# Optimization experiments

Hardware: AMD Instinct MI355X
Metric: run time of the kernel (lower is better)

Reference implementation:

```python
import jax, jax.numpy as jnp
import numpy as np

NS, NV = 48, 10                    # scalar / vector multiplicities (cfg.ns, cfg.nv)
WN = NS * NS + NS * NV             # per-edge TP weight numel: paths 0e*0e->0e and 0e*1o->1o
OUT = NS + 3 * NV                  # out irreps 48x0e + 10x1o -> 78 dims
INV = float(1.0 / np.sqrt(NS))     # e3nn-style path normalization (fan_in = mul_in)
N_LIG, N_REC, N_ATOM = 2000, 2000, 15000
E_LL, E_RR, E_AA = 15000, 10000, 15000
E_LR, E_LA, E_AR = 5000, 8000, 8000


def setup_inputs() -> dict:
    key = jax.random.key(0)
    ks = jax.random.split(key, 40)
    f = lambda i, shape, s=1.0: jax.random.normal(ks[i], shape, dtype=jnp.float32) * s
    ii = lambda i, n, e: jax.random.randint(ks[i], (e,), 0, n, dtype=jnp.int32)
    w_s = (1.0 / (3 * NS)) ** 0.5
    return {
        'lig_x': f(0, (N_LIG, NS)), 'rec_x': f(1, (N_REC, NS)), 'atom_x': f(2, (N_ATOM, NS)),
        'll_attr': f(3, (E_LL, NS)), 'rr_attr': f(4, (E_RR, NS)), 'aa_attr': f(5, (E_AA, NS)),
        'lr_attr': f(6, (E_LR, NS)), 'la_attr': f(7, (E_LA, NS)), 'ar_attr': f(8, (E_AR, NS)),
        'll_sh': f(9, (E_LL, 9)), 'rr_sh': f(10, (E_RR, 9)), 'aa_sh': f(11, (E_AA, 9)),
        'lr_sh': f(12, (E_LR, 9)), 'la_sh': f(13, (E_LA, 9)), 'ar_sh': f(14, (E_AR, 9)),
        'mlp_w1': f(15, (9, 3 * NS, 3 * NS), w_s), 'mlp_b1': jnp.zeros((9, 3 * NS), jnp.float32),
        'mlp_w2': f(16, (9, 3 * NS, 3 * NS), w_s), 'mlp_b2': jnp.zeros((9, 3 * NS), jnp.float32),
        'mlp_w3': f(17, (9, 3 * NS, WN), w_s), 'mlp_b3': jnp.zeros((9, WN), jnp.float32),
        'll_src': ii(18, N_LIG, E_LL), 'll_dst': ii(19, N_LIG, E_LL),
        'rr_src': ii(20, N_REC, E_RR), 'rr_dst': ii(21, N_REC, E_RR),
        'aa_src': ii(22, N_ATOM, E_AA), 'aa_dst': ii(23, N_ATOM, E_AA),
        'lr_lig': ii(24, N_LIG, E_LR), 'lr_rec': ii(25, N_REC, E_LR),
        'la_lig': ii(26, N_LIG, E_LA), 'la_atom': ii(27, N_ATOM, E_LA),
        'ar_atom': ii(28, N_ATOM, E_AR), 'ar_rec': ii(29, N_REC, E_AR),
    }


def _tp_conv(src_x, dst_x, e_attr, e_sh, src_idx, dst_idx, n_dst, w1, b1, w2, b2, w3, b3):
    """FullyConnectedTensorProductConv: per-edge MLP -> TP weights, CG tensor
    product of gathered source features with edge SH, mean scatter to dst."""
    fs = src_x[src_idx]                                          # (E, ns) gather
    z = jnp.concatenate([e_attr, fs, dst_x[dst_idx]], axis=-1)
    h = jax.nn.relu(z @ w1 + b1)
    h = jax.nn.relu(h @ w2 + b2)
    w = h @ w3 + b3                                              # (E, WN) edge-conditioned TP weights
    w0 = w[:, : NS * NS].reshape(-1, NS, NS)                     # 0e x 0e -> 0e path
    wv = w[:, NS * NS :].reshape(-1, NS, NV)                     # 0e x 1o -> 1o path
    out0 = jnp.einsum('ei,eio->eo', fs, w0) * e_sh[:, :1] * INV  # (E, ns)
    outv = jnp.einsum('ei,eiv,em->evm', fs, wv, e_sh[:, 1:4]) * INV  # (E, nv, 3)
    msg = jnp.concatenate([out0, outv.reshape(-1, NV * 3)], axis=-1)
    agg = jax.ops.segment_sum(msg, dst_idx, num_segments=n_dst)
    deg = jax.ops.segment_sum(jnp.ones((msg.shape[0], 1), msg.dtype), dst_idx, num_segments=n_dst)
    return agg / jnp.maximum(deg, 1.0)                           # mean reduction


def reference(lig_x, rec_x, atom_x, ll_attr, rr_attr, aa_attr, lr_attr, la_attr, ar_attr,
              ll_sh, rr_sh, aa_sh, lr_sh, la_sh, ar_sh,
              mlp_w1, mlp_b1, mlp_w2, mlp_b2, mlp_w3, mlp_b3,
              ll_src, ll_dst, rr_src, rr_dst, aa_src, aa_dst,
              lr_lig, lr_rec, la_lig, la_atom, ar_atom, ar_rec):
    P = lambda c: (mlp_w1[c], mlp_b1[c], mlp_w2[c], mlp_b2[c], mlp_w3[c], mlp_b3[c])
    # one interaction layer = 9 structurally distinct convs (lig/rec/atom intra + 6 cross dirs)
    lig_u = (_tp_conv(lig_x, lig_x, ll_attr, ll_sh, ll_src, ll_dst, N_LIG, *P(0))
           + _tp_conv(rec_x, lig_x, lr_attr, lr_sh, lr_rec, lr_lig, N_LIG, *P(1))
           + _tp_conv(atom_x, lig_x, la_attr, la_sh, la_atom, la_lig, N_LIG, *P(2)))
    rec_u = (_tp_conv(lig_x, rec_x, lr_attr, lr_sh, lr_lig, lr_rec, N_REC, *P(3))
           + _tp_conv(rec_x, rec_x, rr_attr, rr_sh, rr_src, rr_dst, N_REC, *P(4))
           + _tp_conv(atom_x, rec_x, ar_attr, ar_sh, ar_atom, ar_rec, N_REC, *P(5)))
    atom_u = (_tp_conv(lig_x, atom_x, la_attr, la_sh, la_lig, la_atom, N_ATOM, *P(6))
            + _tp_conv(rec_x, atom_x, ar_attr, ar_sh, ar_rec, ar_atom, N_ATOM, *P(7))
            + _tp_conv(atom_x, atom_x, aa_attr, aa_sh, aa_src, aa_dst, N_ATOM, *P(8)))
    pad = lambda x: jnp.pad(x, ((0, 0), (0, OUT - NS)))          # residual: pad scalars to out irreps
    return jnp.concatenate([pad(lig_x) + lig_u, pad(rec_x) + rec_u, pad(atom_x) + atom_u], axis=0)
```

## Files before the change

### kernel.cpp

```cpp
#include <hip/hip_runtime.h>


namespace {

constexpr int NCONV = 9;
constexpr int ETOT  = 82000;
constexpr float INV = 0.14433756729740643f;

constexpr int EC[NCONV]     = {15000,5000,8000,5000,10000,8000,8000,8000,15000};
constexpr int NBLKC[NCONV]  = {118,40,63,40,79,63,63,63,118};
constexpr int EOFF[NCONV]   = {0,15000,20000,28000,33000,43000,51000,59000,67000};
constexpr int DEGOFF[NCONV] = {0,2000,4000,6000,8000,10000,12000,27000,42000};
constexpr int NODEC[NCONV]  = {2000,2000,2000,2000,2000,2000,15000,15000,15000};
constexpr int NBLK_TOT = 647;

typedef _Float16 f16;
typedef __attribute__((ext_vector_type(8))) _Float16 f16x8;
typedef __attribute__((ext_vector_type(4))) _Float16 f16x4;
typedef __attribute__((ext_vector_type(4))) float f32x4;

#define MFMA(a, b, c) __builtin_amdgcn_mfma_f32_16x16x32_f16((a), (b), (c), 0, 0, 0)

struct ConvPtrs {
  const float* src_x[NCONV];
  const float* dst_x[NCONV];
  const float* attr[NCONV];
  const float* sh[NCONV];
  const int*   sidx[NCONV];
  const int*   didx[NCONV];
};

}

__device__ __forceinline__ int SW(int idx) { return idx ^ ((idx >> 3) & 3); }

__device__ __forceinline__ int xcd_remap(int bid) {
  const int xcd = bid & 7, slot = bid >> 3;
  return (xcd <= 6) ? (xcd * 81 + slot) : (567 + slot);
}

__device__ __forceinline__ int conv_decode(int bid, int& rem) {
  int c = 0; rem = bid;
  while (c < NCONV - 1 && rem >= NBLKC[c]) { rem -= NBLKC[c]; ++c; }
  return c;
}

__device__ __forceinline__ void gld_lds16(const void* g, void* l) {
  __builtin_amdgcn_global_load_lds(
      (const __attribute__((address_space(1))) void*)g,
      (__attribute__((address_space(3))) void*)l, 16, 0, 0);
}

__global__ __launch_bounds__(256) void prep_all(
    ConvPtrs P,
    const float* __restrict__ w1, const float* __restrict__ b1,
    const float* __restrict__ w2, const float* __restrict__ b2,
    const float* __restrict__ w3, const float* __restrict__ b3,
    f16* __restrict__ w1f, f16* __restrict__ w2f, f16* __restrict__ w3f,
    float* __restrict__ deg) {
  __shared__ float W[145][60];
  const int blk = blockIdx.x;
  if (blk < 203) {
    const int unit = blk * 4 + (threadIdx.x >> 6);
    if (unit >= 810) return;
    const int l = threadIdx.x & 63;
    const int sel = unit >= 405, bb = sel ? unit - 405 : unit;
    const int c = bb / 45, r2 = bb % 45, cb = r2 / 5, s = r2 % 5;
    const float* w  = sel ? w2 : w1;
    const float* bi = sel ? b2 : b1;
    f16* dst = (sel ? w2f : w1f) + ((size_t)(c * 9 + cb) * 5 + s) * 512;
    const int n = cb * 16 + (l & 15);
    f16x8 pack;
#pragma unroll
    for (int j = 0; j < 8; ++j) {
      const int k = s * 32 + ((l >> 4) << 3) + j;
      float v = 0.f;
      if (k < 144)       v = w[((size_t)c * 144 + k) * 144 + n];
      else if (k == 144) v = bi[c * 144 + n];
      pack[j] = (f16)v;
    }
    ((f16x8*)dst)[l] = pack;
  } else if (blk < 635) {
    const int b = blk - 203;
    const int c = b / 48, i = b % 48;
    const float* wc = w3 + (size_t)c * 144 * 2784;
    const float* bc = b3 + (size_t)c * 2784;
    for (int u = threadIdx.x; u < 145 * 58; u += 256) {
      const int row = u / 58, t = u - row * 58;
      const int col = (t < 48) ? (i * 48 + t) : (2304 + i * 10 + (t - 48));
      const float* src = (row == 144) ? bc : (wc + (size_t)row * 2784);
      W[row][t] = src[col];
    }
    __syncthreads();
    f16* dst = w3f + (size_t)(c * 48 + i) * 20 * 512;
#pragma unroll
    for (int it = 0; it < 5; ++it) {
      const int f8 = it * 256 + threadIdx.x;
      const int s = f8 >> 8, g2 = f8 & 255, cb = g2 >> 6, l = g2 & 63;
      const int k0 = s * 32 + ((l >> 4) << 3);
      const int col = cb * 16 + (l & 15);
      f16x8 pack;
#pragma unroll
      for (int j = 0; j < 8; ++j) {
        const int k = k0 + j;
        pack[j] = (f16)((k <= 144 && col < 58) ? W[k][col] : 0.f);
      }
      ((f16x8*)dst)[f8] = pack;
    }
  } else {
    const int gid = (blk - 635) * 256 + threadIdx.x;
    if (gid >= ETOT) return;
    int c = 0;
    while (c < NCONV - 1 && gid >= EOFF[c + 1]) ++c;
    const int e = gid - EOFF[c];
    atomicAdd(&deg[DEGOFF[c] + P.didx[c][e]], 1.0f);
  }
}

__global__ __launch_bounds__(256) void scan_kernel(
    const float* __restrict__ deg, int* __restrict__ offs, int* __restrict__ cursor) {
  __shared__ int part[256];
  const int c = blockIdx.x, N = NODEC[c], base = DEGOFF[c];
  const int tid = threadIdx.x;
  const int chunk = (N + 255) / 256;
  const int start = tid * chunk;
  const int end = (start + chunk < N) ? (start + chunk) : N;
  int s = 0;
  for (int i = start; i < end; ++i) s += (int)deg[base + i];
  part[tid] = s;
  __syncthreads();
  if (tid == 0) {
    int acc = 0;
    for (int k = 0; k < 256; ++k) { int t = part[k]; part[k] = acc; acc += t; }
  }
  __syncthreads();
  int acc = part[tid];
  for (int i = start; i < end; ++i) {
    offs[base + i] = acc; cursor[base + i] = acc;
    acc += (int)deg[base + i];
  }
}

__global__ __launch_bounds__(256) void slot_kernel(
    ConvPtrs P, int* __restrict__ cursor, int* __restrict__ inv_slot) {
  const int gid = blockIdx.x * 256 + threadIdx.x;
  if (gid >= ETOT) return;
  int c = 0;
  while (c < NCONV - 1 && gid >= EOFF[c + 1]) ++c;
  const int e = gid - EOFF[c];
  const int d = P.didx[c][e];
  inv_slot[gid] = atomicAdd(&cursor[DEGOFF[c] + d], 1);
}

template<int NCB, int CB0>
__device__ __forceinline__ void layer_mm(
    const f16x8* __restrict__ Av, const f16x8* __restrict__ wv,
    int c, int lane, int lane_sw, int wr, f32x4 acc[4][5]) {
#pragma unroll
  for (int rb = 0; rb < 4; ++rb)
#pragma unroll
    for (int cb = 0; cb < NCB; ++cb) acc[rb][cb] = (f32x4)0.0f;
#pragma unroll
  for (int s = 0; s < 5; ++s) {
    f16x8 B[NCB];
#pragma unroll
    for (int cb = 0; cb < NCB; ++cb)
      B[cb] = wv[((size_t)(c * 9 + CB0 + cb) * 5 + s) * 64 + lane];
    f16x8 A[4];
#pragma unroll
    for (int rb = 0; rb < 4; ++rb) A[rb] = Av[((wr * 4 + rb) * 5 + s) * 64 + lane_sw];
#pragma unroll
    for (int rb = 0; rb < 4; ++rb)
#pragma unroll
      for (int cb = 0; cb < NCB; ++cb)
        acc[rb][cb] = MFMA(A[rb], B[cb], acc[rb][cb]);
  }
}

template<int NCB, int CB0>
__device__ __forceinline__ void layer_wb(const f32x4 acc[4][5], f16* __restrict__ At,
                                         int lane, int wr) {
#pragma unroll
  for (int cb = 0; cb < NCB; ++cb) {
    const int k = (CB0 + cb) * 16 + (lane & 15);
    const int s = k >> 5, g = (k >> 3) & 3, j = k & 7;
#pragma unroll
    for (int rb = 0; rb < 4; ++rb)
#pragma unroll
      for (int r = 0; r < 4; ++r) {
        const int row = ((lane >> 4) << 2) + r;
        const int sf = (wr * 4 + rb) * 5 + s;
        At[(sf * 64 + SW(g * 16 + row)) * 8 + j] =
            (f16)fmaxf(acc[rb][cb][r], 0.f);
      }
  }
}

__global__ __launch_bounds__(256)
__attribute__((amdgpu_waves_per_eu(3, 3)))
void mlp_kernel(
    ConvPtrs P, const f16* __restrict__ w1f, const f16* __restrict__ w2f,
    f16* __restrict__ h2g, f16* __restrict__ fstg) {
  __shared__ __align__(16) char smem[54272];
  f16* Atile = (f16*)smem;
  f16 (*fst)[48] = (f16 (*)[48])(smem + 40960);
  int* sidb = (int*)(smem + 53248);
  int* dstb = (int*)(smem + 53760);

  const int f = xcd_remap(blockIdx.x);
  int rem; const int c = conv_decode(f, rem);
  const int E = EC[c], e0 = rem * 128;
  const int tid = threadIdx.x, lane = tid & 63, w = tid >> 6;
  const int wr = w >> 1, wc = w & 1;
  const int lane_sw = SW(lane);

  if (tid < 128) {
    int ec = e0 + tid; if (ec >= E) ec = E - 1;
    sidb[tid] = P.sidx[c][ec];
    dstb[tid] = P.didx[c][ec];
  }
  __syncthreads();

  {
    const float* attr = P.attr[c];
    const float* sx = P.src_x[c];
    const float* dx = P.dst_x[c];
#pragma unroll
    for (int it = 0; it < 10; ++it) {
      const int u = it * 256 + tid, j8 = u >> 7, e = u & 127;
      int ec = e0 + e; if (ec >= E) ec = E - 1;
      const float* p;
      if (j8 < 6)       p = attr + (size_t)ec * 48 + j8 * 8;
      else if (j8 < 12) p = sx + (size_t)sidb[e] * 48 + (j8 - 6) * 8;
      else if (j8 < 18) p = dx + (size_t)dstb[e] * 48 + (j8 - 12) * 8;
      else              p = attr;
      const f32x4 va = *(const f32x4*)p;
      const f32x4 vb = *(const f32x4*)(p + 4);
      float v[8];
#pragma unroll
      for (int t = 0; t < 4; ++t) { v[t] = va[t]; v[4 + t] = vb[t]; }
      if (j8 == 18) {
        v[0] = 1.f;
#pragma unroll
        for (int t = 1; t < 8; ++t) v[t] = 0.f;
      } else if (j8 == 19) {
#pragma unroll
        for (int t = 0; t < 8; ++t) v[t] = 0.f;
      }
      f16x8 h;
#pragma unroll
      for (int t = 0; t < 8; ++t) h[t] = (f16)v[t];
      if (j8 >= 6 && j8 < 12) {
        *(f16x8*)&fst[e][(j8 - 6) * 8] = h;
      }
      const int s = j8 >> 2, g = j8 & 3, rbg = e >> 4, row = e & 15;
      ((f16x8*)Atile)[(rbg * 5 + s) * 64 + SW(g * 16 + row)] = h;
    }
  }
  __syncthreads();

  const f16x8* Av = (const f16x8*)Atile;
  f32x4 acc[4][5];
  if (wc == 0) layer_mm<5, 0>(Av, (const f16x8*)w1f, c, lane, lane_sw, wr, acc);
  else         layer_mm<4, 5>(Av, (const f16x8*)w1f, c, lane, lane_sw, wr, acc);
  __syncthreads();
  if (wc == 0) layer_wb<5, 0>(acc, Atile, lane, wr);
  else         layer_wb<4, 5>(acc, Atile, lane, wr);
  __syncthreads();
  if (wc == 0) layer_mm<5, 0>(Av, (const f16x8*)w2f, c, lane, lane_sw, wr, acc);
  else         layer_mm<4, 5>(Av, (const f16x8*)w2f, c, lane, lane_sw, wr, acc);
  __syncthreads();
  if (wc == 0) layer_wb<5, 0>(acc, Atile, lane, wr);
  else         layer_wb<4, 5>(acc, Atile, lane, wr);
  __syncthreads();

  const f16x8* As = (const f16x8*)Atile;
  f16x8* hd = (f16x8*)(h2g + (size_t)f * 20480);
#pragma unroll
  for (int t = 0; t < 10; ++t) hd[t * 256 + tid] = As[t * 256 + tid];
  const f16x8* fs8 = (const f16x8*)fst;
  f16x8* fd = (f16x8*)(fstg + (size_t)f * 6144);
#pragma unroll
  for (int t = 0; t < 3; ++t) fd[t * 256 + tid] = fs8[t * 256 + tid];
}

__device__ __forceinline__ void bilin_step2(
    const f16* __restrict__ slot, const f16 (*fstl)[48], int i,
    const f16x8 Af[4][5], f32x4 msg[4][2], int lane, int wr, int wc) {
  f16x8 fsv[4];
#pragma unroll
  for (int rb = 0; rb < 4; ++rb) {
    const f16 fs = fstl[(wr * 4 + rb) * 16 + (lane & 15)][i];
#pragma unroll
    for (int t = 0; t < 8; ++t) fsv[rb][t] = fs;
  }
  const f16x8* bv = (const f16x8*)slot;
  __builtin_amdgcn_s_setprio(1);
#pragma unroll
  for (int s = 0; s < 5; ++s) {
    const f16x8 Bf0 = bv[(s * 4 + wc * 2 + 0) * 64 + lane];
    const f16x8 Bf1 = bv[(s * 4 + wc * 2 + 1) * 64 + lane];
#pragma unroll
    for (int rb = 0; rb < 4; ++rb) {
      const f16x8 a = Af[rb][s] * fsv[rb];
      msg[rb][0] = MFMA(a, Bf0, msg[rb][0]);
      msg[rb][1] = MFMA(a, Bf1, msg[rb][1]);
    }
  }
  __builtin_amdgcn_s_setprio(0);
}

__global__ __launch_bounds__(256)
__attribute__((amdgpu_waves_per_eu(3, 3)))
void bilin_kernel(
    ConvPtrs P, const f16* __restrict__ w3f, const f16* __restrict__ h2g,
    const f16* __restrict__ fstg, const float* __restrict__ deg,
    const int* __restrict__ inv_slot, f16* __restrict__ medge) {
  __shared__ __align__(16) char smem[53248];
  f16* ring = (f16*)smem;
  f16 (*fstl)[48] = (f16 (*)[48])(smem + 40960);

  const int f = xcd_remap(blockIdx.x);
  int rem; const int c = conv_decode(f, rem);
  const int E = EC[c], e0 = rem * 128;
  const int tid = threadIdx.x, lane = tid & 63, w = tid >> 6;
  const int wr = w >> 1, wc = w & 1;
  const int lane_sw = SW(lane);

  const f16x8* hv = (const f16x8*)(h2g + (size_t)f * 20480);
  f16x8 Af[4][5];
#pragma unroll
  for (int rb = 0; rb < 4; ++rb)
#pragma unroll
    for (int s = 0; s < 5; ++s)
      Af[rb][s] = hv[((wr * 4 + rb) * 5 + s) * 64 + lane_sw];

  const f16* fsrc = fstg + (size_t)f * 6144;
#pragma unroll
  for (int t = 0; t < 3; ++t) {
    const int chunk = w * 3 + t;
    gld_lds16(fsrc + chunk * 512 + lane * 8, ((f16*)fstl) + chunk * 512);
  }
  const f16* __restrict__ w3c = w3f + (size_t)(c * 48) * 10240;
#pragma unroll
  for (int q = 0; q < 5; ++q) {
    const int chunk = q * 4 + w;
    gld_lds16(w3c + chunk * 512 + lane * 8, ring + chunk * 512);
  }

  f32x4 msg[4][2];
#pragma unroll
  for (int rb = 0; rb < 4; ++rb)
#pragma unroll
    for (int cb = 0; cb < 2; ++cb) msg[rb][cb] = (f32x4)0.0f;

#pragma unroll 1
  for (int i = 0; i < 47; ++i) {
    __builtin_amdgcn_s_barrier();
    const f16* gsrc = w3c + (size_t)(i + 1) * 10240;
    f16* bdst = ring + ((i + 1) & 1) * 10240;
#pragma unroll
    for (int q = 0; q < 5; ++q) {
      const int chunk = q * 4 + w;
      gld_lds16(gsrc + chunk * 512 + lane * 8, bdst + chunk * 512);
    }
    asm volatile("s_waitcnt vmcnt(5)" ::: "memory");
    __builtin_amdgcn_s_barrier();
    __builtin_amdgcn_sched_barrier(0);
    bilin_step2(ring + (i & 1) * 10240, fstl, i, Af, msg, lane, wr, wc);
  }
  __builtin_amdgcn_s_barrier();
  asm volatile("s_waitcnt vmcnt(0)" ::: "memory");
  __builtin_amdgcn_s_barrier();
  bilin_step2(ring + (47 & 1) * 10240, fstl, 47, Af, msg, lane, wr, wc);

  const float* __restrict__ shp = P.sh[c];
  const float* __restrict__ degc = deg + DEGOFF[c];
  const int* __restrict__ didx = P.didx[c];
#pragma unroll
  for (int rb = 0; rb < 4; ++rb)
#pragma unroll
    for (int r = 0; r < 4; ++r) {
      const int el = wr * 64 + rb * 16 + ((lane >> 4) << 2) + r;
      const int ec = e0 + el;
      if (ec >= E) continue;
      const float sc = INV / fmaxf(degc[didx[ec]], 1.f);
      const float* shq = shp + (size_t)ec * 9;
      const float s0 = shq[0], s1 = shq[1], s2 = shq[2], s3 = shq[3];
      const int pos = inv_slot[EOFF[c] + ec];
      f16* mp = medge + (size_t)(EOFF[c] + pos) * 80;
#pragma unroll
      for (int cb = 0; cb < 2; ++cb) {
        const int col = (wc * 2 + cb) * 16 + (lane & 15);
        const float v = msg[rb][cb][r] * sc;
        if (col < 48) {
          mp[col] = (f16)(v * s0);
        } else if (col < 58) {
          const int vv = col - 48;
          mp[48 + vv * 3 + 0] = (f16)(v * s1);
          mp[48 + vv * 3 + 1] = (f16)(v * s2);
          mp[48 + vv * 3 + 2] = (f16)(v * s3);
        }
      }
    }
}

__global__ __launch_bounds__(256) void finalize_kernel(
    const float* __restrict__ lig, const float* __restrict__ rec,
    const float* __restrict__ atom, const int* __restrict__ offs,
    const int* __restrict__ cursor, const f16* __restrict__ medge,
    float* __restrict__ out) {
  const int tid = threadIdx.x;
  if (tid >= 240) return;
  const int r3 = tid / 80, j = tid - r3 * 80;
  const int row = blockIdx.x * 3 + r3;
  if (row >= 19000 || j >= 78) return;
  int node, cb; const float* x;
  if (row < 2000)      { node = row;        cb = 0; x = lig; }
  else if (row < 4000) { node = row - 2000; cb = 3; x = rec; }
  else                 { node = row - 4000; cb = 6; x = atom; }
  float r = (j < 48) ? x[(size_t)node * 48 + j] : 0.f;
#pragma unroll
  for (int t = 0; t < 3; ++t) {
    const int c = cb + t;
    const int base = DEGOFF[c] + node;
    const int o = offs[base], e = cursor[base];
    for (int k = o; k < e; ++k)
      r += (float)medge[(size_t)(EOFF[c] + k) * 80 + j];
  }
  out[(size_t)row * 78 + j] = r;
}

extern "C" void kernel_launch(void* const* d_in, const int* in_sizes, int n_in,
                              void* d_out, int out_size, void* d_ws, size_t ws_size,
                              hipStream_t stream) {
  (void)in_sizes; (void)n_in; (void)out_size; (void)ws_size;
  const float* lig_x  = (const float*)d_in[0];
  const float* rec_x  = (const float*)d_in[1];
  const float* atom_x = (const float*)d_in[2];
  const float* attr_ll = (const float*)d_in[3];
  const float* attr_rr = (const float*)d_in[4];
  const float* attr_aa = (const float*)d_in[5];
  const float* attr_lr = (const float*)d_in[6];
  const float* attr_la = (const float*)d_in[7];
  const float* attr_ar = (const float*)d_in[8];
  const float* sh_ll = (const float*)d_in[9];
  const float* sh_rr = (const float*)d_in[10];
  const float* sh_aa = (const float*)d_in[11];
  const float* sh_lr = (const float*)d_in[12];
  const float* sh_la = (const float*)d_in[13];
  const float* sh_ar = (const float*)d_in[14];
  const float* w1 = (const float*)d_in[15];
  const float* b1 = (const float*)d_in[16];
  const float* w2 = (const float*)d_in[17];
  const float* b2 = (const float*)d_in[18];
  const float* w3 = (const float*)d_in[19];
  const float* b3 = (const float*)d_in[20];
  const int* ll_src = (const int*)d_in[21];
  const int* ll_dst = (const int*)d_in[22];
  const int* rr_src = (const int*)d_in[23];
  const int* rr_dst = (const int*)d_in[24];
  const int* aa_src = (const int*)d_in[25];
  const int* aa_dst = (const int*)d_in[26];
  const int* lr_lig = (const int*)d_in[27];
  const int* lr_rec = (const int*)d_in[28];
  const int* la_lig = (const int*)d_in[29];
  const int* la_atom = (const int*)d_in[30];
  const int* ar_atom = (const int*)d_in[31];
  const int* ar_rec  = (const int*)d_in[32];

  f16* w1f = (f16*)d_ws;
  f16* w2f = w1f + 207360;
  f16* w3f = w2f + 207360;
  float* deg     = (float*)(w3f + 4423680);
  int*   offs    = (int*)(deg + 57000);
  int*   cursor  = offs + 57000;
  int*   inv_slot= cursor + 57000;
  f16*   medge   = (f16*)(inv_slot + 82000);
  f16*   h2g     = medge + 6560000;
  f16*   fstg    = h2g + 13250560;

  ConvPtrs P;
  const float* SX[NCONV] = {lig_x, rec_x, atom_x, lig_x, rec_x, atom_x, lig_x, rec_x, atom_x};
  const float* DX[NCONV] = {lig_x, lig_x, lig_x, rec_x, rec_x, rec_x, atom_x, atom_x, atom_x};
  const float* AT[NCONV] = {attr_ll, attr_lr, attr_la, attr_lr, attr_rr, attr_ar, attr_la, attr_ar, attr_aa};
  const float* SH[NCONV] = {sh_ll, sh_lr, sh_la, sh_lr, sh_rr, sh_ar, sh_la, sh_ar, sh_aa};
  const int*   SI[NCONV] = {ll_src, lr_rec, la_atom, lr_lig, rr_src, ar_atom, la_lig, ar_rec, aa_src};
  const int*   DI[NCONV] = {ll_dst, lr_lig, la_lig, lr_rec, rr_dst, ar_rec, la_atom, ar_atom, aa_dst};
  for (int cc = 0; cc < NCONV; ++cc) {
    P.src_x[cc] = SX[cc]; P.dst_x[cc] = DX[cc]; P.attr[cc] = AT[cc];
    P.sh[cc] = SH[cc]; P.sidx[cc] = SI[cc]; P.didx[cc] = DI[cc];
  }

  hipMemsetAsync(deg, 0, 57000 * sizeof(float), stream);
  prep_all<<<956, 256, 0, stream>>>(P, w1, b1, w2, b2, w3, b3, w1f, w2f, w3f, deg);
  scan_kernel<<<NCONV, 256, 0, stream>>>(deg, offs, cursor);
  slot_kernel<<<(ETOT + 255) / 256, 256, 0, stream>>>(P, cursor, inv_slot);
  mlp_kernel<<<NBLK_TOT, 256, 0, stream>>>(P, w1f, w2f, h2g, fstg);
  bilin_kernel<<<NBLK_TOT, 256, 0, stream>>>(P, w3f, h2g, fstg, deg, inv_slot, medge);
  finalize_kernel<<<(19000 + 2) / 3, 256, 0, stream>>>(lig_x, rec_x, atom_x, offs,
                                                       cursor, medge, (float*)d_out);
}
```

Before: 193.0 us.

## Merge pairs of bilinear tiles into 512-thread blocks sharing the W3 ring

The bilinear kernel now processes two 128-edge tiles per 512-thread block, so each streamed 48-slice W3 weight ring in LDS serves 256 edges instead of 128. This halves the number of blocks and the global/L2 traffic for W3 loads. Only five waves issue the async loads, and the rest wait on vmcnt(0). LDS per block rises to 64 KB and waves_per_eu changes to 4, which alters occupancy. The odd-count tail reuses a duplicated tile index, and the hidden epilogue must handle it correctly.

```diff
diff --git a/kernel.cpp b/kernel.cpp
--- a/kernel.cpp
+++ b/kernel.cpp
@@ -9,14 +9,16 @@
 
 constexpr int EC[NCONV]     = {15000,5000,8000,5000,10000,8000,8000,8000,15000};
 constexpr int NBLKC[NCONV]  = {118,40,63,40,79,63,63,63,118};
+constexpr int TOFF[NCONV]   = {0,118,158,221,261,340,403,466,529};
+constexpr int NBLKC2[NCONV] = {59,20,32,20,40,32,32,32,59};
 constexpr int EOFF[NCONV]   = {0,15000,20000,28000,33000,43000,51000,59000,67000};
 constexpr int DEGOFF[NCONV] = {0,2000,4000,6000,8000,10000,12000,27000,42000};
 constexpr int NODEC[NCONV]  = {2000,2000,2000,2000,2000,2000,15000,15000,15000};
 constexpr int NBLK_TOT = 647;
+constexpr int NBLK2_TOT = 326;
 
 typedef _Float16 f16;
 typedef __attribute__((ext_vector_type(8))) _Float16 f16x8;
-typedef __attribute__((ext_vector_type(4))) _Float16 f16x4;
 typedef __attribute__((ext_vector_type(4))) float f32x4;
 
 #define MFMA(a, b, c) __builtin_amdgcn_mfma_f32_16x16x32_f16((a), (b), (c), 0, 0, 0)
@@ -38,10 +40,19 @@
   const int xcd = bid & 7, slot = bid >> 3;
   return (xcd <= 6) ? (xcd * 81 + slot) : (567 + slot);
 }
+__device__ __forceinline__ int xcd_remap326(int bid) {
+  const int xcd = bid & 7, slot = bid >> 3;
+  return (xcd < 6) ? (xcd * 41 + slot) : (246 + (xcd - 6) * 40 + slot);
+}
 
 __device__ __forceinline__ int conv_decode(int bid, int& rem) {
   int c = 0; rem = bid;
   while (c < NCONV - 1 && rem >= NBLKC[c]) { rem -= NBLKC[c]; ++c; }
+  return c;
+}
+__device__ __forceinline__ int conv_decode2(int bid, int& rem) {
+  int c = 0; rem = bid;
+  while (c < NCONV - 1 && rem >= NBLKC2[c]) { rem -= NBLKC2[c]; ++c; }
   return c;
 }
 
@@ -290,7 +301,7 @@
   f16x8 fsv[4];
 #pragma unroll
   for (int rb = 0; rb < 4; ++rb) {
-    const f16 fs = fstl[(wr * 4 + rb) * 16 + (lane & 15)][i];
+    const f16 fs = fstl[wr * 64 + rb * 16 + (lane & 15)][i];
 #pragma unroll
     for (int t = 0; t < 8; ++t) fsv[rb][t] = fs;
   }
@@ -310,42 +321,51 @@
   __builtin_amdgcn_s_setprio(0);
 }
 
-__global__ __launch_bounds__(256)
-__attribute__((amdgpu_waves_per_eu(3, 3)))
+__global__ __launch_bounds__(512)
+__attribute__((amdgpu_waves_per_eu(4, 4)))
 void bilin_kernel(
     ConvPtrs P, const f16* __restrict__ w3f, const f16* __restrict__ h2g,
     const f16* __restrict__ fstg, const float* __restrict__ deg,
     const int* __restrict__ inv_slot, f16* __restrict__ medge) {
-  __shared__ __align__(16) char smem[53248];
+  __shared__ __align__(16) char smem[65536];
   f16* ring = (f16*)smem;
   f16 (*fstl)[48] = (f16 (*)[48])(smem + 40960);
 
-  const int f = xcd_remap(blockIdx.x);
-  int rem; const int c = conv_decode(f, rem);
-  const int E = EC[c], e0 = rem * 128;
+  const int fb = xcd_remap326(blockIdx.x);
+  int rem; const int c = conv_decode2(fb, rem);
+  const int E = EC[c], e0 = rem * 256;
   const int tid = threadIdx.x, lane = tid & 63, w = tid >> 6;
   const int wr = w >> 1, wc = w & 1;
   const int lane_sw = SW(lane);
 
-  const f16x8* hv = (const f16x8*)(h2g + (size_t)f * 20480);
+  const int tcnt = NBLKC[c];
+  const int tg0 = TOFF[c] + 2 * rem;
+  const int tg1 = TOFF[c] + ((2 * rem + 1 < tcnt) ? (2 * rem + 1) : (tcnt - 1));
+  const int tgw = (wr >> 1) ? tg1 : tg0;
+  const int hb  = wr & 1;
+
+  const f16x8* hv = (const f16x8*)(h2g + (size_t)tgw * 20480);
   f16x8 Af[4][5];
 #pragma unroll
   for (int rb = 0; rb < 4; ++rb)
 #pragma unroll
     for (int s = 0; s < 5; ++s)
-      Af[rb][s] = hv[((wr * 4 + rb) * 5 + s) * 64 + lane_sw];
-
-  const f16* fsrc = fstg + (size_t)f * 6144;
+      Af[rb][s] = hv[((hb * 4 + rb) * 5 + s) * 64 + lane_sw];
+
 #pragma unroll
   for (int t = 0; t < 3; ++t) {
     const int chunk = w * 3 + t;
-    gld_lds16(fsrc + chunk * 512 + lane * 8, ((f16*)fstl) + chunk * 512);
+    const int tg = (chunk >= 12) ? tg1 : tg0;
+    const f16* src = fstg + (size_t)tg * 6144 + (chunk % 12) * 512;
+    gld_lds16(src + lane * 8, ((f16*)fstl) + chunk * 512);
   }
   const f16* __restrict__ w3c = w3f + (size_t)(c * 48) * 10240;
-#pragma unroll
-  for (int q = 0; q < 5; ++q) {
-    const int chunk = q * 4 + w;
-    gld_lds16(w3c + chunk * 512 + lane * 8, ring + chunk * 512);
+  if (w < 5) {
+#pragma unroll
+    for (int q = 0; q < 4; ++q) {
+      const int chunk = w * 4 + q;
+      gld_lds16(w3c + chunk * 512 + lane * 8, ring + chunk * 512);
+    }
   }
 
   f32x4 msg[4][2];
@@ -357,14 +377,18 @@
 #pragma unroll 1
   for (int i = 0; i < 47; ++i) {
     __builtin_amdgcn_s_barrier();
-    const f16* gsrc = w3c + (size_t)(i + 1) * 10240;
-    f16* bdst = ring + ((i + 1) & 1) * 10240;
-#pragma unroll
-    for (int q = 0; q < 5; ++q) {
-      const int chunk = q * 4 + w;
-      gld_lds16(gsrc + chunk * 512 + lane * 8, bdst + chunk * 512);
-    }
-    asm volatile("s_waitcnt vmcnt(5)" ::: "memory");
+    if (w < 5) {
+      const f16* gsrc = w3c + (size_t)(i + 1) * 10240;
+      f16* bdst = ring + ((i + 1) & 1) * 10240;
+#pragma unroll
+      for (int q = 0; q < 4; ++q) {
+        const int chunk = w * 4 + q;
+        gld_lds16(gsrc + chunk * 512 + lane * 8, bdst + chunk * 512);
+      }
+      asm volatile("s_waitcnt vmcnt(4)" ::: "memory");
+    } else {
+      asm volatile("s_waitcnt vmcnt(0)" ::: "memory");
+    }
     __builtin_amdgcn_s_barrier();
     __builtin_amdgcn_sched_barrier(0);
     bilin_step2(ring + (i & 1) * 10240, fstl, i, Af, msg, lane, wr, wc);
@@ -497,7 +521,7 @@
   scan_kernel<<<NCONV, 256, 0, stream>>>(deg, offs, cursor);
   slot_kernel<<<(ETOT + 255) / 256, 256, 0, stream>>>(P, cursor, inv_slot);
   mlp_kernel<<<NBLK_TOT, 256, 0, stream>>>(P, w1f, w2f, h2g, fstg);
-  bilin_kernel<<<NBLK_TOT, 256, 0, stream>>>(P, w3f, h2g, fstg, deg, inv_slot, medge);
+  bilin_kernel<<<NBLK2_TOT, 512, 0, stream>>>(P, w3f, h2g, fstg, deg, inv_slot, medge);
   finalize_kernel<<<(19000 + 2) / 3, 256, 0, stream>>>(lig_x, rec_x, atom_x, offs,
                                                        cursor, medge, (float*)d_out);
 }
```

After: 219.9 us. 13.9% more time.

## Load bilinear weight fragments directly from global instead of LDS ring

Applied to the files above, without the earlier changes.

Replaces the double-buffered LDS ring, which staged per-step w3 weight slices with async global-to-LDS copies and barriers, with direct per-wave global loads of the B fragments into registers, unrolled by two. This drops the per-iteration block barriers and most LDS usage, which should raise achievable occupancy. The waves_per_eu pin is also removed. The trade is that latency hiding now relies on the compiler's unrolled loads and cache hits, and each wave now fetches its weight slice from global/L2 itself rather than through the shared LDS copy.

```diff
diff --git a/kernel.cpp b/kernel.cpp
--- a/kernel.cpp
+++ b/kernel.cpp
@@ -16,7 +16,6 @@
 
 typedef _Float16 f16;
 typedef __attribute__((ext_vector_type(8))) _Float16 f16x8;
-typedef __attribute__((ext_vector_type(4))) _Float16 f16x4;
 typedef __attribute__((ext_vector_type(4))) float f32x4;
 
 #define MFMA(a, b, c) __builtin_amdgcn_mfma_f32_16x16x32_f16((a), (b), (c), 0, 0, 0)
@@ -284,41 +283,12 @@
   for (int t = 0; t < 3; ++t) fd[t * 256 + tid] = fs8[t * 256 + tid];
 }
 
-__device__ __forceinline__ void bilin_step2(
-    const f16* __restrict__ slot, const f16 (*fstl)[48], int i,
-    const f16x8 Af[4][5], f32x4 msg[4][2], int lane, int wr, int wc) {
-  f16x8 fsv[4];
-#pragma unroll
-  for (int rb = 0; rb < 4; ++rb) {
-    const f16 fs = fstl[(wr * 4 + rb) * 16 + (lane & 15)][i];
-#pragma unroll
-    for (int t = 0; t < 8; ++t) fsv[rb][t] = fs;
-  }
-  const f16x8* bv = (const f16x8*)slot;
-  __builtin_amdgcn_s_setprio(1);
-#pragma unroll
-  for (int s = 0; s < 5; ++s) {
-    const f16x8 Bf0 = bv[(s * 4 + wc * 2 + 0) * 64 + lane];
-    const f16x8 Bf1 = bv[(s * 4 + wc * 2 + 1) * 64 + lane];
-#pragma unroll
-    for (int rb = 0; rb < 4; ++rb) {
-      const f16x8 a = Af[rb][s] * fsv[rb];
-      msg[rb][0] = MFMA(a, Bf0, msg[rb][0]);
-      msg[rb][1] = MFMA(a, Bf1, msg[rb][1]);
-    }
-  }
-  __builtin_amdgcn_s_setprio(0);
-}
-
 __global__ __launch_bounds__(256)
-__attribute__((amdgpu_waves_per_eu(3, 3)))
 void bilin_kernel(
     ConvPtrs P, const f16* __restrict__ w3f, const f16* __restrict__ h2g,
     const f16* __restrict__ fstg, const float* __restrict__ deg,
     const int* __restrict__ inv_slot, f16* __restrict__ medge) {
-  __shared__ __align__(16) char smem[53248];
-  f16* ring = (f16*)smem;
-  f16 (*fstl)[48] = (f16 (*)[48])(smem + 40960);
+  __shared__ __align__(16) f16 fstl[128][48];
 
   const int f = xcd_remap(blockIdx.x);
   int rem; const int c = conv_decode(f, rem);
@@ -341,12 +311,7 @@
     const int chunk = w * 3 + t;
     gld_lds16(fsrc + chunk * 512 + lane * 8, ((f16*)fstl) + chunk * 512);
   }
-  const f16* __restrict__ w3c = w3f + (size_t)(c * 48) * 10240;
-#pragma unroll
-  for (int q = 0; q < 5; ++q) {
-    const int chunk = q * 4 + w;
-    gld_lds16(w3c + chunk * 512 + lane * 8, ring + chunk * 512);
-  }
+  __syncthreads();
 
   f32x4 msg[4][2];
 #pragma unroll
@@ -354,25 +319,33 @@
 #pragma unroll
     for (int cb = 0; cb < 2; ++cb) msg[rb][cb] = (f32x4)0.0f;
 
-#pragma unroll 1
-  for (int i = 0; i < 47; ++i) {
-    __builtin_amdgcn_s_barrier();
-    const f16* gsrc = w3c + (size_t)(i + 1) * 10240;
-    f16* bdst = ring + ((i + 1) & 1) * 10240;
-#pragma unroll
-    for (int q = 0; q < 5; ++q) {
-      const int chunk = q * 4 + w;
-      gld_lds16(gsrc + chunk * 512 + lane * 8, bdst + chunk * 512);
-    }
-    asm volatile("s_waitcnt vmcnt(5)" ::: "memory");
-    __builtin_amdgcn_s_barrier();
-    __builtin_amdgcn_sched_barrier(0);
-    bilin_step2(ring + (i & 1) * 10240, fstl, i, Af, msg, lane, wr, wc);
-  }
-  __builtin_amdgcn_s_barrier();
-  asm volatile("s_waitcnt vmcnt(0)" ::: "memory");
-  __builtin_amdgcn_s_barrier();
-  bilin_step2(ring + (47 & 1) * 10240, fstl, 47, Af, msg, lane, wr, wc);
+  const f16x8* __restrict__ bg = (const f16x8*)(w3f + (size_t)(c * 48) * 10240);
+#pragma unroll 2
+  for (int i = 0; i < 48; ++i) {
+    f16x8 B[2][5];
+#pragma unroll
+    for (int s = 0; s < 5; ++s)
+#pragma unroll
+      for (int cb = 0; cb < 2; ++cb)
+        B[cb][s] = bg[i * 1280 + (s * 4 + wc * 2 + cb) * 64 + lane];
+    f16x8 fsv[4];
+#pragma unroll
+    for (int rb = 0; rb < 4; ++rb) {
+      const f16 fs = fstl[(wr * 4 + rb) * 16 + (lane & 15)][i];
+#pragma unroll
+      for (int t = 0; t < 8; ++t) fsv[rb][t] = fs;
+    }
+    __builtin_amdgcn_s_setprio(1);
+#pragma unroll
+    for (int s = 0; s < 5; ++s)
+#pragma unroll
+      for (int rb = 0; rb < 4; ++rb) {
+        const f16x8 a = Af[rb][s] * fsv[rb];
+        msg[rb][0] = MFMA(a, B[0][s], msg[rb][0]);
+        msg[rb][1] = MFMA(a, B[1][s], msg[rb][1]);
+      }
+    __builtin_amdgcn_s_setprio(0);
+  }
 
   const float* __restrict__ shp = P.sh[c];
   const float* __restrict__ degc = deg + DEGOFF[c];
```

Result: slower. 211.4 us (+9.5%).
